# Kernel optimization log

Hardware: AMD Instinct MI355X
Metric: run time of the kernel (lower is better)

The kernel has to match this reference:

```python
import jax, jax.numpy as jnp
import numpy as np

B = 131072      # number of graphs
P = 22          # num_players (pad/truncate target)
F = 14          # num_features
N = B * P       # total nodes
H1, H2 = 256, 128


def setup_inputs() -> dict:
    key = jax.random.key(0)
    ks = jax.random.split(key, 8)
    x = jax.random.normal(ks[0], (N, F), dtype=jnp.float32)
    batch = jnp.sort(jax.random.randint(ks[1], (N,), 0, B, dtype=jnp.int32))
    s1 = 1.0 / np.sqrt(P * F)
    s2 = 1.0 / np.sqrt(H1)
    s3 = 1.0 / np.sqrt(H2)
    W1 = jax.random.uniform(ks[2], (H1, P * F), jnp.float32, -s1, s1)
    b1 = jax.random.uniform(ks[3], (H1,), jnp.float32, -s1, s1)
    W2 = jax.random.uniform(ks[4], (H2, H1), jnp.float32, -s2, s2)
    b2 = jax.random.uniform(ks[5], (H2,), jnp.float32, -s2, s2)
    W3 = jax.random.uniform(ks[6], (P, H2), jnp.float32, -s3, s3)
    b3 = jax.random.uniform(ks[7], (P,), jnp.float32, -s3, s3)
    return {"x": x, "batch": batch, "W1": W1, "b1": b1, "W2": W2, "b2": b2, "W3": W3, "b3": b3}


def _flatten_batch(x, batch):
    # Vectorized equivalent of the per-graph mask/slice/pad loop.
    counts = jax.ops.segment_sum(jnp.ones((N,), jnp.int32), batch, num_segments=B)
    starts = jnp.concatenate([jnp.zeros((1,), jnp.int32), jnp.cumsum(counts)[:-1].astype(jnp.int32)])
    pos = jnp.arange(N, dtype=jnp.int32) - starts[batch]  # position within own graph
    # nodes beyond the first P per graph are truncated -> route to dump slot P
    slot = jnp.where(pos < P, pos, P)
    buf = jnp.zeros((B, P + 1, F), dtype=x.dtype)          # zero padding for short graphs
    buf = buf.at[batch, slot].set(x)
    return buf[:, :P, :].reshape(B, P * F)


def reference(x, batch, W1, b1, W2, b2, W3, b3):
    flat = _flatten_batch(x, batch)                        # [B, 308]
    h1 = jax.nn.relu(flat @ W1.T + b1)                     # dropout is eval-mode identity
    h2 = jax.nn.relu(h1 @ W2.T + b2)
    logits = h2 @ W3.T + b3                                # [B, 22]
    return logits
```

## Files before the change

kernel.cpp:

```cpp
#include <hip/hip_runtime.h>
#include <hip/hip_fp16.h>

typedef __attribute__((ext_vector_type(8))) _Float16 half8;
typedef __attribute__((ext_vector_type(4))) float f32x4;

namespace {
constexpr int B_G = 131072;
constexpr int P   = 22;
constexpr int F   = 14;
constexpr int NF  = 308;
constexpr long long N_NODES = (long long)B_G * P;

constexpr int G    = 64;
constexpr int NBLK = B_G / G;

constexpr int KS1 = 10;
constexpr int KS2 = 8;
constexpr int KS3 = 4;
constexpr int JT1 = 16;
constexpr int JT2 = 8;
constexpr int JT3 = 2;

constexpr int W1F = 0;
constexpr int W2F = W1F + KS1 * JT1 * 1024;
constexpr int W3F = W2F + KS2 * JT2 * 1024;
constexpr int CVT_DWORDS = (KS1*JT1 + KS2*JT2 + KS3*JT3) * 256;
}

__device__ __forceinline__ unsigned short f2h(float v) {
    __half h = __float2half(v);
    return *reinterpret_cast<unsigned short*>(&h);
}

__global__ void convert_w_kernel(const float* __restrict__ W1,
                                 const float* __restrict__ W2,
                                 const float* __restrict__ W3,
                                 unsigned* __restrict__ ws)
{
    int p = blockIdx.x * 256 + threadIdx.x;
    if (p >= CVT_DWORDS) return;
    const int n1 = KS1 * JT1 * 256;
    const int n2 = KS2 * JT2 * 256;
    const float* W; int NK, NJ, stride, JT, oB, pl;
    if (p < n1)            { W = W1; NK = NF;  NJ = 256; stride = NF;  JT = JT1; oB = W1F/4; pl = p; }
    else if (p < n1 + n2)  { W = W2; NK = 256; NJ = 128; stride = 256; JT = JT2; oB = W2F/4; pl = p - n1; }
    else                   { W = W3; NK = 128; NJ = 22;  stride = 128; JT = JT3; oB = W3F/4; pl = p - n1 - n2; }

    const int e2   = pl & 3;
    const int lane = (pl >> 2) & 63;
    const int jt   = (pl >> 8) % JT;
    const int ks   = (pl >> 8) / JT;
    const int j    = jt * 16 + (lane & 15);
    const int kb   = ks * 32 + (lane >> 4) * 8 + e2 * 2;

    unsigned d = 0;
    #pragma unroll
    for (int q = 0; q < 2; ++q) {
        const int k = kb + q;
        const float v = (k < NK && j < NJ) ? W[j * stride + k] : 0.0f;
        d |= (unsigned)f2h(v) << (16 * q);
    }
    ws[oB + pl] = d;
}

#define MFMA16(A_, B_, C_) __builtin_amdgcn_mfma_f32_16x16x32_f16(A_, B_, C_, 0, 0, 0)

#define LOADB1(H_, KS_) { \
    _Pragma("unroll") for (int n = 0; n < 4; ++n) \
        H_[n] = *reinterpret_cast<const half8*>(&B1[((((KS_) * JT1) + (wv * 4 + n)) * 64 + lane) * 8]); }

#define COMP1(H_, KS_) { \
    half8 a_[4]; \
    _Pragma("unroll") for (int m = 0; m < 4; ++m) \
        a_[m] = *reinterpret_cast<const half8*>(&s_scr[(((KS_) * 4 + kq) * G + (m * 16 + r16)) * 8]); \
    _Pragma("unroll") for (int n = 0; n < 4; ++n) \
        _Pragma("unroll") for (int m = 0; m < 4; ++m) \
            acc[m][n] = MFMA16(a_[m], H_[n], acc[m][n]); }

#define LOADB2(H_, KS_) { \
    _Pragma("unroll") for (int n = 0; n < 2; ++n) \
        H_[n] = *reinterpret_cast<const half8*>(&B2[((((KS_) * JT2) + (wv * 2 + n)) * 64 + lane) * 8]); }

#define COMP2(H_, KS_) { \
    half8 a_[4]; \
    _Pragma("unroll") for (int m = 0; m < 4; ++m) \
        a_[m] = *reinterpret_cast<const half8*>(&s_scr[(((KS_) * 4 + kq) * G + (m * 16 + r16)) * 8]); \
    _Pragma("unroll") for (int n = 0; n < 2; ++n) \
        _Pragma("unroll") for (int m = 0; m < 4; ++m) \
            acc2[m][n] = MFMA16(a_[m], H_[n], acc2[m][n]); }

#define GATHER_BODY(I_) { \
    const int gl = batch[I_] - g0; \
    const int pp = (I_) - s_start[gl]; \
    if (pp < P) { \
        const float2* xr = reinterpret_cast<const float2*>(x + (size_t)(I_) * F); \
        _Pragma("unroll") for (int q = 0; q < 7; ++q) { \
            const float2 v = xr[q]; \
            const int k = pp * F + q * 2; \
            const unsigned d = (unsigned)f2h(v.x) | ((unsigned)f2h(v.y) << 16); \
            const int off = (((k >> 5) * 4 + ((k >> 3) & 3)) * G + gl) * 8 + (k & 7); \
            *reinterpret_cast<unsigned*>(&s_scr[off]) = d; \
        } \
    } }

#define PIN8(V_) asm volatile("" :: "v"(V_))

__global__ __launch_bounds__(256, 3)
void mlp_mfma_kernel(const float* __restrict__ x,
                     const int* __restrict__ batch,
                     const float* __restrict__ b1,
                     const float* __restrict__ b2,
                     const float* __restrict__ b3,
                     const unsigned short* __restrict__ ws,
                     float* __restrict__ out)
{
    __shared__ __align__(16) unsigned short s_scr[24576];
    __shared__ float s_b1[256], s_b2[128], s_b3[32];
    __shared__ int s_start[G + 1];

    const int t    = threadIdx.x;
    const int g0   = blockIdx.x * G;
    const int lane = t & 63;
    const int wv   = t >> 6;
    const int r16  = lane & 15;
    const int kq   = lane >> 4;

    s_b1[t] = b1[t];
    if (t < 128) s_b2[t] = b2[t];
    if (t < 32)  s_b3[t] = (t < 22) ? b3[t] : 0.0f;

    if (t <= G) {
        const int target = g0 + t;
        long long wl = (long long)target * P - 5001; if (wl < 0) wl = 0;
        long long wh = (long long)target * P + 5001; if (wh > N_NODES) wh = N_NODES;
        int lo = (int)wl, hi = (int)wh;
        while (lo < hi) { int mid = (lo + hi) >> 1; if (batch[mid] < target) lo = mid + 1; else hi = mid; }
        const bool ok = (lo == 0 || batch[lo - 1] < target) &&
                        (lo == (int)N_NODES || batch[lo] >= target);
        if (!ok) {
            lo = 0; hi = (int)N_NODES;
            while (lo < hi) { int mid = (lo + hi) >> 1; if (batch[mid] < target) lo = mid + 1; else hi = mid; }
        }
        s_start[t] = lo;
    }

    for (int i = t; i < 2560; i += 256)
        reinterpret_cast<uint4*>(s_scr)[i] = make_uint4(0u, 0u, 0u, 0u);

    const unsigned short* B1 = ws + W1F / 2;
    const unsigned short* B2 = ws + W2F / 2;
    const unsigned short* B3 = ws + W3F / 2;

    half8 Ba[4], Bb[4], Bc[4];
    LOADB1(Ba, 0)
    LOADB1(Bb, 1)
    LOADB1(Bc, 2)
    __syncthreads();

    const int s0 = s_start[0], s1 = s_start[G];
    #pragma unroll
    for (int u = 0; u < 7; ++u) {
        const int i = s0 + t + u * 256;
        if (i < s1) GATHER_BODY(i)
    }
    for (int i = s0 + t + 7 * 256; i < s1; i += 256)
        GATHER_BODY(i)

    PIN8(Ba[0]); PIN8(Ba[1]); PIN8(Ba[2]); PIN8(Ba[3]);
    PIN8(Bb[0]); PIN8(Bb[1]); PIN8(Bb[2]); PIN8(Bb[3]);
    PIN8(Bc[0]); PIN8(Bc[1]); PIN8(Bc[2]); PIN8(Bc[3]);
    __syncthreads();

    f32x4 acc[4][4];
    #pragma unroll
    for (int m = 0; m < 4; ++m)
        #pragma unroll
        for (int n = 0; n < 4; ++n) acc[m][n] = (f32x4){0.f, 0.f, 0.f, 0.f};

    COMP1(Ba, 0)  LOADB1(Ba, 3)
    COMP1(Bb, 1)  LOADB1(Bb, 4)
    COMP1(Bc, 2)  LOADB1(Bc, 5)
    COMP1(Ba, 3)  LOADB1(Ba, 6)
    COMP1(Bb, 4)  LOADB1(Bb, 7)
    COMP1(Bc, 5)  LOADB1(Bc, 8)
    COMP1(Ba, 6)  LOADB1(Ba, 9)
    COMP1(Bb, 7)

    half8 Ca[2], Cb[2], Cc[2];
    LOADB2(Ca, 0)
    LOADB2(Cb, 1)
    LOADB2(Cc, 2)
    COMP1(Bc, 8)
    COMP1(Ba, 9)
    __syncthreads();

    #pragma unroll
    for (int n = 0; n < 4; ++n) {
        const int j = (wv * 4 + n) * 16 + r16;
        const float bb = s_b1[j];
        const int base = (((j >> 5) * 4 + ((j >> 3) & 3)) * G) * 8 + (j & 7);
        #pragma unroll
        for (int m = 0; m < 4; ++m)
            #pragma unroll
            for (int r = 0; r < 4; ++r) {
                const int g = m * 16 + kq * 4 + r;
                s_scr[base + g * 8] = f2h(fmaxf(acc[m][n][r] + bb, 0.0f));
            }
    }
    __syncthreads();

    f32x4 acc2[4][2];
    #pragma unroll
    for (int m = 0; m < 4; ++m)
        #pragma unroll
        for (int n = 0; n < 2; ++n) acc2[m][n] = (f32x4){0.f, 0.f, 0.f, 0.f};

    COMP2(Ca, 0)  LOADB2(Ca, 3)
    COMP2(Cb, 1)  LOADB2(Cb, 4)
    COMP2(Cc, 2)  LOADB2(Cc, 5)
    COMP2(Ca, 3)  LOADB2(Ca, 6)
    COMP2(Cb, 4)  LOADB2(Cb, 7)
    COMP2(Cc, 5)
    COMP2(Ca, 6)

    half8 D3[8];
    #pragma unroll
    for (int ks = 0; ks < KS3; ++ks)
        #pragma unroll
        for (int n = 0; n < 2; ++n)
            D3[ks * 2 + n] = *reinterpret_cast<const half8*>(&B3[((ks * JT3 + n) * 64 + lane) * 8]);
    COMP2(Cb, 7)

    #pragma unroll
    for (int n = 0; n < 2; ++n) {
        const int j = (wv * 2 + n) * 16 + r16;
        const float bb = s_b2[j];
        const int base = 16384 + (((j >> 5) * 4 + ((j >> 3) & 3)) * G) * 8 + (j & 7);
        #pragma unroll
        for (int m = 0; m < 4; ++m)
            #pragma unroll
            for (int r = 0; r < 4; ++r) {
                const int g = m * 16 + kq * 4 + r;
                s_scr[base + g * 8] = f2h(fmaxf(acc2[m][n][r] + bb, 0.0f));
            }
    }
    __syncthreads();

    {
        f32x4 acc3[2];
        acc3[0] = (f32x4){0.f, 0.f, 0.f, 0.f};
        acc3[1] = (f32x4){0.f, 0.f, 0.f, 0.f};
        #pragma unroll
        for (int ks = 0; ks < KS3; ++ks) {
            const half8 a = *reinterpret_cast<const half8*>(
                &s_scr[16384 + ((ks * 4 + kq) * G + (wv * 16 + r16)) * 8]);
            #pragma unroll
            for (int n = 0; n < 2; ++n)
                acc3[n] = MFMA16(a, D3[ks * 2 + n], acc3[n]);
        }
        #pragma unroll
        for (int n = 0; n < 2; ++n) {
            const int j = n * 16 + r16;
            if (j < P) {
                const float bb = s_b3[j];
                #pragma unroll
                for (int r = 0; r < 4; ++r) {
                    const int g = wv * 16 + kq * 4 + r;
                    out[(size_t)(g0 + g) * P + j] = acc3[n][r] + bb;
                }
            }
        }
    }
}

extern "C" void kernel_launch(void* const* d_in, const int* in_sizes, int n_in,
                              void* d_out, int out_size, void* d_ws, size_t ws_size,
                              hipStream_t stream) {
    const float* x     = (const float*)d_in[0];
    const int*   batch = (const int*)  d_in[1];
    const float* W1    = (const float*)d_in[2];
    const float* b1    = (const float*)d_in[3];
    const float* W2    = (const float*)d_in[4];
    const float* b2    = (const float*)d_in[5];
    const float* W3    = (const float*)d_in[6];
    const float* b3    = (const float*)d_in[7];
    float* out = (float*)d_out;

    convert_w_kernel<<<dim3((CVT_DWORDS + 255) / 256), dim3(256), 0, stream>>>(
        W1, W2, W3, (unsigned*)d_ws);
    mlp_mfma_kernel<<<dim3(NBLK), dim3(256), 0, stream>>>(
        x, batch, b1, b2, b3, (const unsigned short*)d_ws, out);
}
```

Baseline: 68.43 us.

## Stage MLP weights through double-buffered LDS via async global-to-LDS loads

Weights for all three layers are now copied from global memory into two alternating LDS buffers with global_load_lds, instead of being held in registers through a triple-buffered direct-load pipeline. Each k-slice is prefetched into one buffer while the other is consumed by MFMAs, with a vmcnt wait and barrier after every step. The aim is to cut register pressure and redundant per-wave global loads. In exchange, LDS use grows (occupancy hint drops from 3 to 2 blocks per CU) and a block-wide barrier is added per k-step.

```diff
diff --git a/kernel.cpp b/kernel.cpp
--- a/kernel.cpp
+++ b/kernel.cpp
@@ -25,6 +25,10 @@
 constexpr int W2F = W1F + KS1 * JT1 * 1024;
 constexpr int W3F = W2F + KS2 * JT2 * 1024;
 constexpr int CVT_DWORDS = (KS1*JT1 + KS2*JT2 + KS3*JT3) * 256;
+
+constexpr int WB0 = 20480;
+constexpr int WB1 = 28672;
+constexpr int LDS_USH = 36864;
 }
 
 __device__ __forceinline__ unsigned short f2h(float v) {
@@ -63,31 +67,50 @@
     ws[oB + pl] = d;
 }
 
+__device__ __forceinline__ void gload_lds16(const void* g, void* l) {
+    __builtin_amdgcn_global_load_lds(
+        (const __attribute__((address_space(1))) unsigned int*)g,
+        (__attribute__((address_space(3))) unsigned int*)l, 16, 0, 0);
+}
+
 #define MFMA16(A_, B_, C_) __builtin_amdgcn_mfma_f32_16x16x32_f16(A_, B_, C_, 0, 0, 0)
 
-#define LOADB1(H_, KS_) { \
+#define STAGE_W1(KS_, BUF_) { \
+    const char* gsrc = ws8 + W1F + (KS_) * 16384; \
+    _Pragma("unroll") for (int r = 0; r < 4; ++r) \
+        gload_lds16(gsrc + (r * 256 + t) * 16, &s_lds[(BUF_) + (r * 256 + t) * 8]); }
+
+#define STAGE_W2(KS_, BUF_) { \
+    const char* gsrc = ws8 + W2F + (KS_) * 8192; \
+    _Pragma("unroll") for (int r = 0; r < 2; ++r) \
+        gload_lds16(gsrc + (r * 256 + t) * 16, &s_lds[(BUF_) + (r * 256 + t) * 8]); }
+
+#define STAGE_W3(BUF_) { \
+    const char* gsrc = ws8 + W3F; \
+    _Pragma("unroll") for (int r = 0; r < 2; ++r) \
+        gload_lds16(gsrc + (r * 256 + t) * 16, &s_lds[(BUF_) + (r * 256 + t) * 8]); }
+
+#define VWBAR() { asm volatile("s_waitcnt vmcnt(0)" ::: "memory"); __syncthreads(); }
+
+#define COMP1L(KS_, BUF_) { \
+    half8 a_[4], b_[4]; \
+    _Pragma("unroll") for (int m = 0; m < 4; ++m) \
+        a_[m] = *reinterpret_cast<const half8*>(&s_lds[(((KS_) * 4 + kq) * G + (m * 16 + r16)) * 8]); \
     _Pragma("unroll") for (int n = 0; n < 4; ++n) \
-        H_[n] = *reinterpret_cast<const half8*>(&B1[((((KS_) * JT1) + (wv * 4 + n)) * 64 + lane) * 8]); }
-
-#define COMP1(H_, KS_) { \
-    half8 a_[4]; \
-    _Pragma("unroll") for (int m = 0; m < 4; ++m) \
-        a_[m] = *reinterpret_cast<const half8*>(&s_scr[(((KS_) * 4 + kq) * G + (m * 16 + r16)) * 8]); \
+        b_[n] = *reinterpret_cast<const half8*>(&s_lds[(BUF_) + (((wv * 4 + n) * 64) + lane) * 8]); \
     _Pragma("unroll") for (int n = 0; n < 4; ++n) \
         _Pragma("unroll") for (int m = 0; m < 4; ++m) \
-            acc[m][n] = MFMA16(a_[m], H_[n], acc[m][n]); }
-
-#define LOADB2(H_, KS_) { \
+            acc[m][n] = MFMA16(a_[m], b_[n], acc[m][n]); }
+
+#define COMP2L(KS_, BUF_) { \
+    half8 a_[4], b_[2]; \
+    _Pragma("unroll") for (int m = 0; m < 4; ++m) \
+        a_[m] = *reinterpret_cast<const half8*>(&s_lds[(((KS_) * 4 + kq) * G + (m * 16 + r16)) * 8]); \
     _Pragma("unroll") for (int n = 0; n < 2; ++n) \
-        H_[n] = *reinterpret_cast<const half8*>(&B2[((((KS_) * JT2) + (wv * 2 + n)) * 64 + lane) * 8]); }
-
-#define COMP2(H_, KS_) { \
-    half8 a_[4]; \
-    _Pragma("unroll") for (int m = 0; m < 4; ++m) \
-        a_[m] = *reinterpret_cast<const half8*>(&s_scr[(((KS_) * 4 + kq) * G + (m * 16 + r16)) * 8]); \
+        b_[n] = *reinterpret_cast<const half8*>(&s_lds[(BUF_) + (((wv * 2 + n) * 64) + lane) * 8]); \
     _Pragma("unroll") for (int n = 0; n < 2; ++n) \
         _Pragma("unroll") for (int m = 0; m < 4; ++m) \
-            acc2[m][n] = MFMA16(a_[m], H_[n], acc2[m][n]); }
+            acc2[m][n] = MFMA16(a_[m], b_[n], acc2[m][n]); }
 
 #define GATHER_BODY(I_) { \
     const int gl = batch[I_] - g0; \
@@ -99,13 +122,11 @@
             const int k = pp * F + q * 2; \
             const unsigned d = (unsigned)f2h(v.x) | ((unsigned)f2h(v.y) << 16); \
             const int off = (((k >> 5) * 4 + ((k >> 3) & 3)) * G + gl) * 8 + (k & 7); \
-            *reinterpret_cast<unsigned*>(&s_scr[off]) = d; \
+            *reinterpret_cast<unsigned*>(&s_lds[off]) = d; \
         } \
     } }
 
-#define PIN8(V_) asm volatile("" :: "v"(V_))
-
-__global__ __launch_bounds__(256, 3)
+__global__ __launch_bounds__(256, 2)
 void mlp_mfma_kernel(const float* __restrict__ x,
                      const int* __restrict__ batch,
                      const float* __restrict__ b1,
@@ -114,7 +135,7 @@
                      const unsigned short* __restrict__ ws,
                      float* __restrict__ out)
 {
-    __shared__ __align__(16) unsigned short s_scr[24576];
+    __shared__ __align__(16) unsigned short s_lds[LDS_USH];
     __shared__ float s_b1[256], s_b2[128], s_b3[32];
     __shared__ int s_start[G + 1];
 
@@ -124,6 +145,7 @@
     const int wv   = t >> 6;
     const int r16  = lane & 15;
     const int kq   = lane >> 4;
+    const char* ws8 = (const char*)ws;
 
     s_b1[t] = b1[t];
     if (t < 128) s_b2[t] = b2[t];
@@ -145,17 +167,10 @@
     }
 
     for (int i = t; i < 2560; i += 256)
-        reinterpret_cast<uint4*>(s_scr)[i] = make_uint4(0u, 0u, 0u, 0u);
-
-    const unsigned short* B1 = ws + W1F / 2;
-    const unsigned short* B2 = ws + W2F / 2;
-    const unsigned short* B3 = ws + W3F / 2;
-
-    half8 Ba[4], Bb[4], Bc[4];
-    LOADB1(Ba, 0)
-    LOADB1(Bb, 1)
-    LOADB1(Bc, 2)
+        reinterpret_cast<uint4*>(s_lds)[i] = make_uint4(0u, 0u, 0u, 0u);
     __syncthreads();
+
+    STAGE_W1(0, WB0)
 
     const int s0 = s_start[0], s1 = s_start[G];
     #pragma unroll
@@ -165,11 +180,7 @@
     }
     for (int i = s0 + t + 7 * 256; i < s1; i += 256)
         GATHER_BODY(i)
-
-    PIN8(Ba[0]); PIN8(Ba[1]); PIN8(Ba[2]); PIN8(Ba[3]);
-    PIN8(Bb[0]); PIN8(Bb[1]); PIN8(Bb[2]); PIN8(Bb[3]);
-    PIN8(Bc[0]); PIN8(Bc[1]); PIN8(Bc[2]); PIN8(Bc[3]);
-    __syncthreads();
+    VWBAR()
 
     f32x4 acc[4][4];
     #pragma unroll
@@ -177,22 +188,16 @@
         #pragma unroll
         for (int n = 0; n < 4; ++n) acc[m][n] = (f32x4){0.f, 0.f, 0.f, 0.f};
 
-    COMP1(Ba, 0)  LOADB1(Ba, 3)
-    COMP1(Bb, 1)  LOADB1(Bb, 4)
-    COMP1(Bc, 2)  LOADB1(Bc, 5)
-    COMP1(Ba, 3)  LOADB1(Ba, 6)
-    COMP1(Bb, 4)  LOADB1(Bb, 7)
-    COMP1(Bc, 5)  LOADB1(Bc, 8)
-    COMP1(Ba, 6)  LOADB1(Ba, 9)
-    COMP1(Bb, 7)
-
-    half8 Ca[2], Cb[2], Cc[2];
-    LOADB2(Ca, 0)
-    LOADB2(Cb, 1)
-    LOADB2(Cc, 2)
-    COMP1(Bc, 8)
-    COMP1(Ba, 9)
-    __syncthreads();
+    STAGE_W1(1, WB1)  COMP1L(0, WB0)  VWBAR()
+    STAGE_W1(2, WB0)  COMP1L(1, WB1)  VWBAR()
+    STAGE_W1(3, WB1)  COMP1L(2, WB0)  VWBAR()
+    STAGE_W1(4, WB0)  COMP1L(3, WB1)  VWBAR()
+    STAGE_W1(5, WB1)  COMP1L(4, WB0)  VWBAR()
+    STAGE_W1(6, WB0)  COMP1L(5, WB1)  VWBAR()
+    STAGE_W1(7, WB1)  COMP1L(6, WB0)  VWBAR()
+    STAGE_W1(8, WB0)  COMP1L(7, WB1)  VWBAR()
+    STAGE_W1(9, WB1)  COMP1L(8, WB0)  VWBAR()
+    STAGE_W2(0, WB0)  COMP1L(9, WB1)  VWBAR()
 
     #pragma unroll
     for (int n = 0; n < 4; ++n) {
@@ -204,7 +209,7 @@
             #pragma unroll
             for (int r = 0; r < 4; ++r) {
                 const int g = m * 16 + kq * 4 + r;
-                s_scr[base + g * 8] = f2h(fmaxf(acc[m][n][r] + bb, 0.0f));
+                s_lds[base + g * 8] = f2h(fmaxf(acc[m][n][r] + bb, 0.0f));
             }
     }
     __syncthreads();
@@ -215,33 +220,26 @@
         #pragma unroll
         for (int n = 0; n < 2; ++n) acc2[m][n] = (f32x4){0.f, 0.f, 0.f, 0.f};
 
-    COMP2(Ca, 0)  LOADB2(Ca, 3)
-    COMP2(Cb, 1)  LOADB2(Cb, 4)
-    COMP2(Cc, 2)  LOADB2(Cc, 5)
-    COMP2(Ca, 3)  LOADB2(Ca, 6)
-    COMP2(Cb, 4)  LOADB2(Cb, 7)
-    COMP2(Cc, 5)
-    COMP2(Ca, 6)
-
-    half8 D3[8];
-    #pragma unroll
-    for (int ks = 0; ks < KS3; ++ks)
-        #pragma unroll
-        for (int n = 0; n < 2; ++n)
-            D3[ks * 2 + n] = *reinterpret_cast<const half8*>(&B3[((ks * JT3 + n) * 64 + lane) * 8]);
-    COMP2(Cb, 7)
+    STAGE_W2(1, WB1)  COMP2L(0, WB0)  VWBAR()
+    STAGE_W2(2, WB0)  COMP2L(1, WB1)  VWBAR()
+    STAGE_W2(3, WB1)  COMP2L(2, WB0)  VWBAR()
+    STAGE_W2(4, WB0)  COMP2L(3, WB1)  VWBAR()
+    STAGE_W2(5, WB1)  COMP2L(4, WB0)  VWBAR()
+    STAGE_W2(6, WB0)  COMP2L(5, WB1)  VWBAR()
+    STAGE_W2(7, WB1)  COMP2L(6, WB0)  VWBAR()
+    STAGE_W3(WB0)     COMP2L(7, WB1)  VWBAR()
 
     #pragma unroll
     for (int n = 0; n < 2; ++n) {
         const int j = (wv * 2 + n) * 16 + r16;
         const float bb = s_b2[j];
-        const int base = 16384 + (((j >> 5) * 4 + ((j >> 3) & 3)) * G) * 8 + (j & 7);
+        const int base = WB1 + (((j >> 5) * 4 + ((j >> 3) & 3)) * G) * 8 + (j & 7);
         #pragma unroll
         for (int m = 0; m < 4; ++m)
             #pragma unroll
             for (int r = 0; r < 4; ++r) {
                 const int g = m * 16 + kq * 4 + r;
-                s_scr[base + g * 8] = f2h(fmaxf(acc2[m][n][r] + bb, 0.0f));
+                s_lds[base + g * 8] = f2h(fmaxf(acc2[m][n][r] + bb, 0.0f));
             }
     }
     __syncthreads();
@@ -253,10 +251,13 @@
         #pragma unroll
         for (int ks = 0; ks < KS3; ++ks) {
             const half8 a = *reinterpret_cast<const half8*>(
-                &s_scr[16384 + ((ks * 4 + kq) * G + (wv * 16 + r16)) * 8]);
+                &s_lds[WB1 + ((ks * 4 + kq) * G + (wv * 16 + r16)) * 8]);
             #pragma unroll
-            for (int n = 0; n < 2; ++n)
-                acc3[n] = MFMA16(a, D3[ks * 2 + n], acc3[n]);
+            for (int n = 0; n < 2; ++n) {
+                const half8 b = *reinterpret_cast<const half8*>(
+                    &s_lds[WB0 + ((ks * JT3 + n) * 64 + lane) * 8]);
+                acc3[n] = MFMA16(a, b, acc3[n]);
+            }
         }
         #pragma unroll
         for (int n = 0; n < 2; ++n) {
```

Result: slower. 89.65 us (+31.0%).
